# Kernel optimization log

Hardware: AMD Instinct MI355X
Metric: run time of the kernel (lower is better)

## Reference

```python
import jax, jax.numpy as jnp
import numpy as np

NP, NA = 200000, 100000      # paper / author node counts
E = 1000000                  # edges per relation
DP, DA, H = 128, 64, 32      # paper feat, author feat, hidden


def setup_inputs() -> dict:
    key = jax.random.key(0)
    ks = jax.random.split(key, 22)
    g = lambda k, s: jax.random.normal(k, s, jnp.float32) * 0.05
    z = lambda n: jnp.zeros((n,), jnp.float32)
    return dict(
        x_paper=jax.random.normal(ks[0], (NP, DP), jnp.float32),
        x_author=jax.random.normal(ks[1], (NA, DA), jnp.float32),
        ei_cites=jax.random.randint(ks[2], (2, E), 0, NP),  # paper -> paper
        ei_writes=jnp.stack([jax.random.randint(ks[3], (E,), 0, NA),
                             jax.random.randint(ks[4], (E,), 0, NP)]),  # author -> paper
        ei_rev=jnp.stack([jax.random.randint(ks[5], (E,), 0, NP),
                          jax.random.randint(ks[6], (E,), 0, NA)]),  # paper -> author
        # layer 1 SAGEConv weights per edge type: lin_l (with bias), lin_r (no bias)
        W1l_cites=g(ks[7], (DP, H)), b1l_cites=z(H), W1r_cites=g(ks[8], (DP, H)),
        W1l_writes=g(ks[9], (DA, H)), b1l_writes=z(H), W1r_writes=g(ks[10], (DP, H)),
        W1l_rev=g(ks[11], (DP, H)), b1l_rev=z(H), W1r_rev=g(ks[12], (DA, H)),
        # layer 2
        W2l_cites=g(ks[13], (H, H)), b2l_cites=z(H), W2r_cites=g(ks[14], (H, H)),
        W2l_writes=g(ks[15], (H, H)), b2l_writes=z(H), W2r_writes=g(ks[16], (H, H)),
        W2l_rev=g(ks[17], (H, H)), b2l_rev=z(H), W2r_rev=g(ks[18], (H, H)),
        # head Linear(32, 1)
        Wh=g(ks[19], (H, 1)), bh=z(1),
    )


def _sage(x_src, x_dst, ei, Wl, bl, Wr):
    """SAGEConv: lin_l(mean_{j in N(i)} x_j) + lin_r(x_i)."""
    n_dst = x_dst.shape[0]
    src, dst = ei[0], ei[1]
    msum = jax.ops.segment_sum(x_src[src], dst, num_segments=n_dst)  # [n_dst, d_src]
    cnt = jax.ops.segment_sum(jnp.ones((ei.shape[1],), x_src.dtype), dst,
                              num_segments=n_dst)
    mean = msum / jnp.maximum(cnt, 1.0)[:, None]  # zero-degree rows stay 0
    return mean @ Wl + bl + x_dst @ Wr


def reference(x_paper, x_author, ei_cites, ei_writes, ei_rev,
              W1l_cites, b1l_cites, W1r_cites,
              W1l_writes, b1l_writes, W1r_writes,
              W1l_rev, b1l_rev, W1r_rev,
              W2l_cites, b2l_cites, W2r_cites,
              W2l_writes, b2l_writes, W2r_writes,
              W2l_rev, b2l_rev, W2r_rev,
              Wh, bh):
    # layer 1 (to_hetero: sum over edge types per dst node type), then relu
    p1 = jax.nn.relu(_sage(x_paper, x_paper, ei_cites, W1l_cites, b1l_cites, W1r_cites)
                     + _sage(x_author, x_paper, ei_writes, W1l_writes, b1l_writes, W1r_writes))
    a1 = jax.nn.relu(_sage(x_paper, x_author, ei_rev, W1l_rev, b1l_rev, W1r_rev))
    # layer 2: only the 'paper' output is consumed downstream
    p2 = (_sage(p1, p1, ei_cites, W2l_cites, b2l_cites, W2r_cites)
          + _sage(a1, p1, ei_writes, W2l_writes, b2l_writes, W2r_writes))
    # head: Linear(32, 1); model_config is None -> raw logits
    return p2 @ Wh + bh
```

## Files before the change

kernel.cpp:

```cpp
#include <hip/hip_runtime.h>
#include <hip/hip_bf16.h>


#define SPAN  2048
#define EPT   8
#define NBKT  1563
#define CAP   1024
#define SMASK 0x3FFFF

typedef __bf16 bf16x8 __attribute__((ext_vector_type(8)));
typedef __bf16 bf16x2 __attribute__((ext_vector_type(2)));
typedef float f32x4 __attribute__((ext_vector_type(4)));

__global__ void prep_kernel(const float* W1l_c, const float* W1l_rev,
                            const float* W1r_c, const float* W1r_w,
                            const float* W1l_w, const float* W1r_rev,
                            const float* W2l_c, const float* W2l_w,
                            const float* W2r_c, const float* W2r_w,
                            const float* b2l_c, const float* b2l_w,
                            const float* Wh, const float* bh,
                            __bf16* Bp_t, __bf16* Ba_t, float* uvec, int* gcur) {
    int t = threadIdx.x;
    for (int i = t; i < 3 * NBKT; i += 256) gcur[i] = i << 10;
    for (int idx = t; idx < 96 * 128; idx += 256) {
        int n = idx >> 7, k = idx & 127;
        float v;
        if (n < 32)      v = W1l_c[k * 32 + n];
        else if (n < 64) v = W1l_rev[k * 32 + (n - 32)];
        else             v = W1r_c[k * 32 + (n - 64)] + W1r_w[k * 32 + (n - 64)];
        Bp_t[n * 128 + k] = (__bf16)v;
    }
    for (int idx = t; idx < 64 * 64; idx += 256) {
        int n = idx >> 6, k = idx & 63;
        float v = (n < 32) ? W1l_w[k * 32 + n] : W1r_rev[k * 32 + (n - 32)];
        Ba_t[n * 64 + k] = (__bf16)v;
    }
    if (t < 32) {
        float uc = 0.f, uw = 0.f, ur = 0.f;
        for (int j = 0; j < 32; ++j) {
            float wh = Wh[j];
            uc += W2l_c[t * 32 + j] * wh;
            uw += W2l_w[t * 32 + j] * wh;
            ur += (W2r_c[t * 32 + j] + W2r_w[t * 32 + j]) * wh;
        }
        uvec[t] = uc; uvec[32 + t] = uw; uvec[64 + t] = ur;
        if (t == 0) {
            float c0 = bh[0];
            for (int j = 0; j < 32; ++j) c0 += (b2l_c[j] + b2l_w[j]) * Wh[j];
            uvec[96] = c0;
        }
    }
}

template <int K, int NG>
__device__ __forceinline__ void proj_body(const float* __restrict__ X,
                                          const __bf16* __restrict__ Bt,
                                          __bf16* __restrict__ D0,
                                          __bf16* __restrict__ D1,
                                          __bf16* __restrict__ D2, int M, int bid) {
    constexpr int NT = NG * 2, KT = K / 32;
    int lane = threadIdx.x & 63;
    int wave = (bid * 256 + (int)threadIdx.x) >> 6;
    int m0 = wave * 16;
    if (m0 + 16 > M) return;
    int lr = lane & 15;
    int quad = lane >> 4;

    bf16x8 bfrag[NT][KT];
#pragma unroll
    for (int ct = 0; ct < NT; ++ct)
#pragma unroll
        for (int ks = 0; ks < KT; ++ks)
            bfrag[ct][ks] = *(const bf16x8*)(Bt + (ct * 16 + lr) * K + ks * 32 + quad * 8);

    bf16x8 afrag[KT];
    const float* xrow = X + (size_t)(m0 + lr) * K + quad * 8;
#pragma unroll
    for (int ks = 0; ks < KT; ++ks) {
        f32x4 lo = *(const f32x4*)(xrow + ks * 32);
        f32x4 hi = *(const f32x4*)(xrow + ks * 32 + 4);
        bf16x8 a;
#pragma unroll
        for (int j = 0; j < 4; ++j) { a[j] = (__bf16)lo[j]; a[4 + j] = (__bf16)hi[j]; }
        afrag[ks] = a;
    }

    int odd = lane & 1;
#pragma unroll
    for (int ct = 0; ct < NT; ++ct) {
        f32x4 acc = {0.f, 0.f, 0.f, 0.f};
#pragma unroll
        for (int ks = 0; ks < KT; ++ks)
            acc = __builtin_amdgcn_mfma_f32_16x16x32_bf16(afrag[ks], bfrag[ct][ks], acc, 0, 0, 0);
        __bf16* D = ((ct >> 1) == 0) ? D0 : (((ct >> 1) == 1) ? D1 : D2);
        int col = (ct & 1) * 16 + lr;
        int cw = col & ~1;
        int rbase = m0 + quad * 4;
        float o0 = __shfl_xor(acc[0], 1, 64);
        float o1 = __shfl_xor(acc[1], 1, 64);
        float o2 = __shfl_xor(acc[2], 1, 64);
        float o3 = __shfl_xor(acc[3], 1, 64);
        float s0 = odd ? o2 : acc[0], t0 = odd ? acc[2] : o0;
        float s1 = odd ? o3 : acc[1], t1 = odd ? acc[3] : o1;
        int rb = rbase + odd * 2;
        bf16x2 v0; v0[0] = (__bf16)s0; v0[1] = (__bf16)t0;
        bf16x2 v1; v1[0] = (__bf16)s1; v1[1] = (__bf16)t1;
        *(bf16x2*)(D + (size_t)(rb + 0) * 32 + cw) = v0;
        *(bf16x2*)(D + (size_t)(rb + 1) * 32 + cw) = v1;
    }
}

__device__ void scatter_body(const int* __restrict__ eiC, const int* __restrict__ eiW,
                             const int* __restrict__ eiR, int* __restrict__ gcur,
                             unsigned* __restrict__ ebuf, int E, int npart, int bid,
                             int* cnt) {
    int rel = bid / npart, blk = bid % npart;
    const int* ei = rel == 0 ? eiC : (rel == 1 ? eiW : eiR);
    int shift = (rel == 2) ? 6 : 7;
    unsigned dmask = (1u << shift) - 1;
    int t = threadIdx.x;
    int e0 = blk * SPAN, e1 = min(E, e0 + SPAN);
    for (int i = t; i < NBKT; i += 256) cnt[i] = 0;
    __syncthreads();
    int d8[EPT], s8[EPT];
#pragma unroll
    for (int j = 0; j < EPT; ++j) {
        int e = e0 + t + j * 256;
        if (e < e1) {
            d8[j] = ei[E + e];
            s8[j] = ei[e];
            atomicAdd(&cnt[d8[j] >> shift], 1);
        } else {
            d8[j] = -1;
        }
    }
    __syncthreads();
    for (int i = t; i < NBKT; i += 256) {
        int c = cnt[i];
        cnt[i] = c ? atomicAdd(&gcur[rel * NBKT + i], c) : 0;
    }
    __syncthreads();
#pragma unroll
    for (int j = 0; j < EPT; ++j) {
        if (d8[j] >= 0) {
            int b = d8[j] >> shift;
            int gpos = atomicAdd(&cnt[b], 1);
            if (gpos < (((rel * NBKT + b) + 1) << 10))
                ebuf[gpos] = ((unsigned)(d8[j] & dmask) << 18) | (unsigned)s8[j];
        }
    }
}

__global__ __launch_bounds__(256) void mid_kernel(
    const float* __restrict__ Xp, const float* __restrict__ Xa,
    const __bf16* __restrict__ Bp_t, const __bf16* __restrict__ Ba_t,
    __bf16* __restrict__ YpC, __bf16* __restrict__ YpR, __bf16* __restrict__ YpD,
    __bf16* __restrict__ YaW, __bf16* __restrict__ YaD,
    const int* __restrict__ eiC, const int* __restrict__ eiW,
    const int* __restrict__ eiR, int* __restrict__ gcur,
    unsigned* __restrict__ ebuf, int NP, int NA, int E,
    int nPp, int nPa, int npart) {
    __shared__ int cnt[NBKT];
    int bid = blockIdx.x;
    if (bid < 3 * npart) {
        scatter_body(eiC, eiW, eiR, gcur, ebuf, E, npart, bid, cnt);
        return;
    }
    bid -= 3 * npart;
    if (bid < nPp) { proj_body<128, 3>(Xp, Bp_t, YpC, YpR, YpD, NP, bid); return; }
    bid -= nPp;
    proj_body<64, 2>(Xa, Ba_t, YaW, YaD, nullptr, NA, bid);
}

__global__ __launch_bounds__(256) void sort_kernel(
    unsigned* __restrict__ ebuf, const int* __restrict__ gcur,
    int* __restrict__ nstart, int* __restrict__ ncnt) {
    __shared__ unsigned stage[CAP];
    __shared__ int cnt[128], exc[128], cur[128];
    int idx = blockIdx.x;
    int rel = idx / NBKT, b = idx % NBKT;
    int nodes = (rel == 2) ? 64 : 128;
    int t = threadIdx.x;
    int start = idx << 10;
    int n = min(gcur[idx] - start, CAP);
    if (t < 128) cnt[t] = 0;
    __syncthreads();
    for (int i = t; i < n; i += 256) atomicAdd(&cnt[ebuf[start + i] >> 18], 1);
    __syncthreads();
    if (t < 128) exc[t] = cnt[t];
    __syncthreads();
    for (int d = 1; d < 128; d <<= 1) {
        int v = 0;
        if (t < 128) v = exc[t] + ((t >= d) ? exc[t - d] : 0);
        __syncthreads();
        if (t < 128) exc[t] = v;
        __syncthreads();
    }
    if (t < 128) { int e = exc[t] - cnt[t]; exc[t] = e; cur[t] = e; }
    __syncthreads();
    for (int i = t; i < n; i += 256) {
        unsigned w = ebuf[start + i];
        int pos = atomicAdd(&cur[w >> 18], 1);
        stage[pos] = w & SMASK;
    }
    __syncthreads();
    for (int i = t; i < n; i += 256) ebuf[start + i] = stage[i];
    int nbase = (rel == 0) ? b * 128
              : (rel == 1) ? NBKT * 128 + b * 128
                           : 2 * NBKT * 128 + b * 64;
    if (t < nodes) { nstart[nbase + t] = start + exc[t]; ncnt[nbase + t] = cnt[t]; }
}

__device__ __forceinline__ float2 gather2(const __bf16* __restrict__ S,
                                          const unsigned* __restrict__ ebuf,
                                          int o, int n, int l16, int sub) {
    float x = 0.f, y = 0.f;
    int e = sub;
    for (; e + 6 < n; e += 8) {
        int s0 = ebuf[o + e], s1 = ebuf[o + e + 2];
        int s2 = ebuf[o + e + 4], s3 = ebuf[o + e + 6];
        bf16x2 v0 = *(const bf16x2*)(S + (size_t)s0 * 32 + 2 * l16);
        bf16x2 v1 = *(const bf16x2*)(S + (size_t)s1 * 32 + 2 * l16);
        bf16x2 v2 = *(const bf16x2*)(S + (size_t)s2 * 32 + 2 * l16);
        bf16x2 v3 = *(const bf16x2*)(S + (size_t)s3 * 32 + 2 * l16);
        x += (float)v0[0] + (float)v1[0] + (float)v2[0] + (float)v3[0];
        y += (float)v0[1] + (float)v1[1] + (float)v2[1] + (float)v3[1];
    }
    for (; e < n; e += 2) {
        bf16x2 v = *(const bf16x2*)(S + (size_t)ebuf[o + e] * 32 + 2 * l16);
        x += (float)v[0]; y += (float)v[1];
    }
    x += __shfl_xor(x, 16, 64);
    y += __shfl_xor(y, 16, 64);
    return make_float2(x, y);
}

__global__ __launch_bounds__(256) void agg_kernel(
    const __bf16* __restrict__ YpC, const __bf16* __restrict__ YaW,
    const __bf16* __restrict__ YpD, const __bf16* __restrict__ YpR,
    const __bf16* __restrict__ YaD, const unsigned* __restrict__ ebuf,
    const int* __restrict__ nstart, const int* __restrict__ ncnt,
    const float* __restrict__ b1l_c, const float* __restrict__ b1l_w,
    const float* __restrict__ b1l_r, const float* __restrict__ uvec,
    float* __restrict__ s_c, float* __restrict__ s_r, float* __restrict__ s_w,
    int NP, int NA) {
    int g = (blockIdx.x * 256 + (int)threadIdx.x) >> 5;
    int lane32 = threadIdx.x & 31;
    int l16 = lane32 & 15, sub = lane32 >> 4, c2 = 2 * l16;
    const int NPS = NBKT * 128;
    if (g < NP) {
        int oC = nstart[g], nC = ncnt[g];
        float2 aC = gather2(YpC, ebuf, oC, nC, l16, sub);
        int oW = nstart[NPS + g], nW = ncnt[NPS + g];
        float2 aW = gather2(YaW, ebuf, oW, nW, l16, sub);
        float rC = 1.f / (float)max(nC, 1), rW = 1.f / (float)max(nW, 1);
        bf16x2 d = *(const bf16x2*)(YpD + (size_t)g * 32 + c2);
        float p0 = fmaxf(aC.x * rC + aW.x * rW + (float)d[0] + b1l_c[c2] + b1l_w[c2], 0.f);
        float p1 = fmaxf(aC.y * rC + aW.y * rW + (float)d[1] + b1l_c[c2 + 1] + b1l_w[c2 + 1], 0.f);
        float vc = p0 * uvec[c2] + p1 * uvec[c2 + 1];
        float vr = p0 * uvec[64 + c2] + p1 * uvec[64 + c2 + 1];
        for (int m = 1; m < 16; m <<= 1) {
            vc += __shfl_xor(vc, m, 64); vr += __shfl_xor(vr, m, 64);
        }
        if (lane32 == 0) { s_c[g] = vc; s_r[g] = vr; }
    } else if (g < NP + NA) {
        int ga = g - NP;
        int oR = nstart[2 * NPS + ga], nR = ncnt[2 * NPS + ga];
        float2 aR = gather2(YpR, ebuf, oR, nR, l16, sub);
        float rR = 1.f / (float)max(nR, 1);
        bf16x2 d = *(const bf16x2*)(YaD + (size_t)ga * 32 + c2);
        float p0 = fmaxf(aR.x * rR + (float)d[0] + b1l_r[c2], 0.f);
        float p1 = fmaxf(aR.y * rR + (float)d[1] + b1l_r[c2 + 1], 0.f);
        float vw = p0 * uvec[32 + c2] + p1 * uvec[32 + c2 + 1];
        for (int m = 1; m < 16; m <<= 1) vw += __shfl_xor(vw, m, 64);
        if (lane32 == 0) s_w[ga] = vw;
    }
}

__global__ __launch_bounds__(256) void out_kernel(
    const float* __restrict__ s_c, const float* __restrict__ s_w,
    const float* __restrict__ s_r, const unsigned* __restrict__ ebuf,
    const int* __restrict__ nstart, const int* __restrict__ ncnt,
    const float* __restrict__ uvec, float* __restrict__ out, int NP) {
    int gn = blockIdx.x * 256 + threadIdx.x;
    if (gn >= NP) return;
    const int NPS = NBKT * 128;
    int o = nstart[gn], n = ncnt[gn];
    float sC = 0.f;
    for (int e = 0; e < n; ++e) sC += s_c[ebuf[o + e]];
    int o2 = nstart[NPS + gn], n2 = ncnt[NPS + gn];
    float sW = 0.f;
    for (int e = 0; e < n2; ++e) sW += s_w[ebuf[o2 + e]];
    out[gn] = sC / (float)max(n, 1) + sW / (float)max(n2, 1) + s_r[gn] + uvec[96];
}

extern "C" void kernel_launch(void* const* d_in, const int* in_sizes, int n_in,
                              void* d_out, int out_size, void* d_ws, size_t ws_size,
                              hipStream_t stream) {
    const float* x_paper  = (const float*)d_in[0];
    const float* x_author = (const float*)d_in[1];
    const int* eiC = (const int*)d_in[2];
    const int* eiW = (const int*)d_in[3];
    const int* eiR = (const int*)d_in[4];
    const float* W1l_c  = (const float*)d_in[5];
    const float* b1l_c  = (const float*)d_in[6];
    const float* W1r_c  = (const float*)d_in[7];
    const float* W1l_w  = (const float*)d_in[8];
    const float* b1l_w  = (const float*)d_in[9];
    const float* W1r_w  = (const float*)d_in[10];
    const float* W1l_r  = (const float*)d_in[11];
    const float* b1l_r  = (const float*)d_in[12];
    const float* W1r_r  = (const float*)d_in[13];
    const float* W2l_c  = (const float*)d_in[14];
    const float* b2l_c  = (const float*)d_in[15];
    const float* W2r_c  = (const float*)d_in[16];
    const float* W2l_w  = (const float*)d_in[17];
    const float* b2l_w  = (const float*)d_in[18];
    const float* W2r_w  = (const float*)d_in[19];
    const float* Wh = (const float*)d_in[23];
    const float* bh = (const float*)d_in[24];

    const int NP = in_sizes[0] / 128;
    const int NA = in_sizes[1] / 64;
    const int E  = in_sizes[2] / 2;
    const int npart = (E + SPAN - 1) / SPAN;
    const int nPp = (NP + 63) / 64;
    const int nPa = (NA + 63) / 64;
    const int NNODE = NBKT * 128 * 2 + NBKT * 64;

    char* p = (char*)d_ws;
    auto alloc = [&](size_t bytes) -> void* {
        void* r = (void*)p;
        p += (bytes + 255) & ~(size_t)255;
        return r;
    };
    __bf16* YpC = (__bf16*)alloc((size_t)NP * 32 * 2);
    __bf16* YpR = (__bf16*)alloc((size_t)NP * 32 * 2);
    __bf16* YpD = (__bf16*)alloc((size_t)NP * 32 * 2);
    __bf16* YaW = (__bf16*)alloc((size_t)NA * 32 * 2);
    __bf16* YaD = (__bf16*)alloc((size_t)NA * 32 * 2);
    __bf16* Bp_t = (__bf16*)alloc(96 * 128 * 2);
    __bf16* Ba_t = (__bf16*)alloc(64 * 64 * 2);
    float* uvec = (float*)alloc(128 * 4);
    float* s_c  = (float*)alloc((size_t)NP * 4);
    float* s_r  = (float*)alloc((size_t)NP * 4);
    float* s_w  = (float*)alloc((size_t)NA * 4);
    int* gcur   = (int*)alloc((size_t)3 * NBKT * 4);
    int* nstart = (int*)alloc((size_t)NNODE * 4);
    int* ncnt   = (int*)alloc((size_t)NNODE * 4);
    unsigned* ebuf = (unsigned*)alloc((size_t)3 * NBKT * CAP * 4);

    prep_kernel<<<1, 256, 0, stream>>>(W1l_c, W1l_r, W1r_c, W1r_w, W1l_w, W1r_r,
                                       W2l_c, W2l_w, W2r_c, W2r_w, b2l_c, b2l_w,
                                       Wh, bh, Bp_t, Ba_t, uvec, gcur);

    mid_kernel<<<nPp + nPa + 3 * npart, 256, 0, stream>>>(
        x_paper, x_author, Bp_t, Ba_t, YpC, YpR, YpD, YaW, YaD,
        eiC, eiW, eiR, gcur, ebuf, NP, NA, E, nPp, nPa, npart);

    sort_kernel<<<3 * NBKT, 256, 0, stream>>>(ebuf, gcur, nstart, ncnt);

    agg_kernel<<<((NP + NA) * 32 + 255) / 256, 256, 0, stream>>>(
        YpC, YaW, YpD, YpR, YaD, ebuf, nstart, ncnt,
        b1l_c, b1l_w, b1l_r, uvec, s_c, s_r, s_w, NP, NA);

    out_kernel<<<(NP + 255) / 256, 256, 0, stream>>>(
        s_c, s_w, s_r, ebuf, nstart, ncnt, uvec, (float*)d_out, NP);
}
```

Baseline: 436.1 us.

## Fuse bucket sort with layer-1 aggregation using LDS-resident sorted edge lists

Merges the per-bucket counting sort and the layer-1 gather/aggregate into one kernel. Each block sorts its cites and writes buckets (or one rev bucket) in shared memory and reads neighbor indices straight from LDS instead of re-reading the sorted global edge buffer. The rev relation is no longer written back to global memory because only layer 1 uses it. Gather loops now process four edges per iteration with predicated tails, in both the fused kernel and the final output kernel. This removes one kernel launch and a global round trip of the edge lists, at the cost of 16 lanes per node instead of 32 and lower per-block parallelism.

```diff
diff --git a/kernel.cpp b/kernel.cpp
--- a/kernel.cpp
+++ b/kernel.cpp
@@ -172,108 +172,152 @@
     proj_body<64, 2>(Xa, Ba_t, YaW, YaD, nullptr, NA, bid);
 }
 
-__global__ __launch_bounds__(256) void sort_kernel(
-    unsigned* __restrict__ ebuf, const int* __restrict__ gcur,
-    int* __restrict__ nstart, int* __restrict__ ncnt) {
-    __shared__ unsigned stage[CAP];
-    __shared__ int cnt[128], exc[128], cur[128];
-    int idx = blockIdx.x;
-    int rel = idx / NBKT, b = idx % NBKT;
-    int nodes = (rel == 2) ? 64 : 128;
-    int t = threadIdx.x;
-    int start = idx << 10;
-    int n = min(gcur[idx] - start, CAP);
-    if (t < 128) cnt[t] = 0;
-    __syncthreads();
-    for (int i = t; i < n; i += 256) atomicAdd(&cnt[ebuf[start + i] >> 18], 1);
-    __syncthreads();
-    if (t < 128) exc[t] = cnt[t];
-    __syncthreads();
-    for (int d = 1; d < 128; d <<= 1) {
-        int v = 0;
-        if (t < 128) v = exc[t] + ((t >= d) ? exc[t - d] : 0);
-        __syncthreads();
-        if (t < 128) exc[t] = v;
-        __syncthreads();
-    }
-    if (t < 128) { int e = exc[t] - cnt[t]; exc[t] = e; cur[t] = e; }
-    __syncthreads();
-    for (int i = t; i < n; i += 256) {
-        unsigned w = ebuf[start + i];
-        int pos = atomicAdd(&cur[w >> 18], 1);
-        stage[pos] = w & SMASK;
-    }
-    __syncthreads();
-    for (int i = t; i < n; i += 256) ebuf[start + i] = stage[i];
-    int nbase = (rel == 0) ? b * 128
-              : (rel == 1) ? NBKT * 128 + b * 128
-                           : 2 * NBKT * 128 + b * 64;
-    if (t < nodes) { nstart[nbase + t] = start + exc[t]; ncnt[nbase + t] = cnt[t]; }
-}
-
-__device__ __forceinline__ float2 gather2(const __bf16* __restrict__ S,
-                                          const unsigned* __restrict__ ebuf,
-                                          int o, int n, int l16, int sub) {
+__device__ __forceinline__ float2 gatherL(const __bf16* __restrict__ S,
+                                          const unsigned* __restrict__ lst,
+                                          int o, int n, int l16) {
     float x = 0.f, y = 0.f;
-    int e = sub;
-    for (; e + 6 < n; e += 8) {
-        int s0 = ebuf[o + e], s1 = ebuf[o + e + 2];
-        int s2 = ebuf[o + e + 4], s3 = ebuf[o + e + 6];
+    for (int e = 0; e < n; e += 4) {
+        int m = n - e;
+        unsigned s0 = lst[o + e];
+        unsigned s1 = (m > 1) ? lst[o + e + 1] : s0;
+        unsigned s2 = (m > 2) ? lst[o + e + 2] : s0;
+        unsigned s3 = (m > 3) ? lst[o + e + 3] : s0;
         bf16x2 v0 = *(const bf16x2*)(S + (size_t)s0 * 32 + 2 * l16);
         bf16x2 v1 = *(const bf16x2*)(S + (size_t)s1 * 32 + 2 * l16);
         bf16x2 v2 = *(const bf16x2*)(S + (size_t)s2 * 32 + 2 * l16);
         bf16x2 v3 = *(const bf16x2*)(S + (size_t)s3 * 32 + 2 * l16);
-        x += (float)v0[0] + (float)v1[0] + (float)v2[0] + (float)v3[0];
-        y += (float)v0[1] + (float)v1[1] + (float)v2[1] + (float)v3[1];
-    }
-    for (; e < n; e += 2) {
-        bf16x2 v = *(const bf16x2*)(S + (size_t)ebuf[o + e] * 32 + 2 * l16);
-        x += (float)v[0]; y += (float)v[1];
-    }
-    x += __shfl_xor(x, 16, 64);
-    y += __shfl_xor(y, 16, 64);
+        x += (float)v0[0]; y += (float)v0[1];
+        if (m > 1) { x += (float)v1[0]; y += (float)v1[1]; }
+        if (m > 2) { x += (float)v2[0]; y += (float)v2[1]; }
+        if (m > 3) { x += (float)v3[0]; y += (float)v3[1]; }
+    }
     return make_float2(x, y);
 }
 
-__global__ __launch_bounds__(256) void agg_kernel(
+__global__ __launch_bounds__(256) void sagg_kernel(
     const __bf16* __restrict__ YpC, const __bf16* __restrict__ YaW,
     const __bf16* __restrict__ YpD, const __bf16* __restrict__ YpR,
-    const __bf16* __restrict__ YaD, const unsigned* __restrict__ ebuf,
-    const int* __restrict__ nstart, const int* __restrict__ ncnt,
+    const __bf16* __restrict__ YaD, unsigned* __restrict__ ebuf,
+    const int* __restrict__ gcur, int* __restrict__ nstart, int* __restrict__ ncnt,
     const float* __restrict__ b1l_c, const float* __restrict__ b1l_w,
     const float* __restrict__ b1l_r, const float* __restrict__ uvec,
     float* __restrict__ s_c, float* __restrict__ s_r, float* __restrict__ s_w,
     int NP, int NA) {
-    int g = (blockIdx.x * 256 + (int)threadIdx.x) >> 5;
-    int lane32 = threadIdx.x & 31;
-    int l16 = lane32 & 15, sub = lane32 >> 4, c2 = 2 * l16;
+    __shared__ unsigned S0[CAP], S1[CAP];
+    __shared__ int cnt0[128], exc0[128], cur0[128];
+    __shared__ int cnt1[128], exc1[128], cur1[128];
+    __shared__ int scan[256];
     const int NPS = NBKT * 128;
-    if (g < NP) {
-        int oC = nstart[g], nC = ncnt[g];
-        float2 aC = gather2(YpC, ebuf, oC, nC, l16, sub);
-        int oW = nstart[NPS + g], nW = ncnt[NPS + g];
-        float2 aW = gather2(YaW, ebuf, oW, nW, l16, sub);
-        float rC = 1.f / (float)max(nC, 1), rW = 1.f / (float)max(nW, 1);
-        bf16x2 d = *(const bf16x2*)(YpD + (size_t)g * 32 + c2);
-        float p0 = fmaxf(aC.x * rC + aW.x * rW + (float)d[0] + b1l_c[c2] + b1l_w[c2], 0.f);
-        float p1 = fmaxf(aC.y * rC + aW.y * rW + (float)d[1] + b1l_c[c2 + 1] + b1l_w[c2 + 1], 0.f);
-        float vc = p0 * uvec[c2] + p1 * uvec[c2 + 1];
-        float vr = p0 * uvec[64 + c2] + p1 * uvec[64 + c2 + 1];
-        for (int m = 1; m < 16; m <<= 1) {
-            vc += __shfl_xor(vc, m, 64); vr += __shfl_xor(vr, m, 64);
-        }
-        if (lane32 == 0) { s_c[g] = vc; s_r[g] = vr; }
-    } else if (g < NP + NA) {
-        int ga = g - NP;
-        int oR = nstart[2 * NPS + ga], nR = ncnt[2 * NPS + ga];
-        float2 aR = gather2(YpR, ebuf, oR, nR, l16, sub);
-        float rR = 1.f / (float)max(nR, 1);
-        bf16x2 d = *(const bf16x2*)(YaD + (size_t)ga * 32 + c2);
-        float p0 = fmaxf(aR.x * rR + (float)d[0] + b1l_r[c2], 0.f);
-        float p1 = fmaxf(aR.y * rR + (float)d[1] + b1l_r[c2 + 1], 0.f);
-        float vw = p0 * uvec[32 + c2] + p1 * uvec[32 + c2 + 1];
-        for (int m = 1; m < 16; m <<= 1) vw += __shfl_xor(vw, m, 64);
-        if (lane32 == 0) s_w[ga] = vw;
+    int t = threadIdx.x;
+    int sg = t >> 4, l16 = t & 15, c2 = 2 * l16;
+    int bid = blockIdx.x;
+
+    if (bid < NBKT) {
+        int b = bid;
+        int i0 = b, i1 = NBKT + b;
+        int st0 = i0 << 10, st1 = i1 << 10;
+        int n0 = min(gcur[i0] - st0, CAP), n1 = min(gcur[i1] - st1, CAP);
+        if (t < 128) { cnt0[t] = 0; cnt1[t] = 0; }
+        __syncthreads();
+        for (int i = t; i < n0; i += 256) atomicAdd(&cnt0[ebuf[st0 + i] >> 18], 1);
+        for (int i = t; i < n1; i += 256) atomicAdd(&cnt1[ebuf[st1 + i] >> 18], 1);
+        __syncthreads();
+        int own = (t < 128) ? cnt0[t] : cnt1[t - 128];
+        scan[t] = own;
+        __syncthreads();
+        for (int d = 1; d < 128; d <<= 1) {
+            int nv = scan[t] + (((t & 127) >= d) ? scan[t - d] : 0);
+            __syncthreads();
+            scan[t] = nv;
+            __syncthreads();
+        }
+        int excl = scan[t] - own;
+        if (t < 128) { exc0[t] = excl; cur0[t] = excl; }
+        else         { exc1[t - 128] = excl; cur1[t - 128] = excl; }
+        __syncthreads();
+        for (int i = t; i < n0; i += 256) {
+            unsigned w = ebuf[st0 + i];
+            int pos = atomicAdd(&cur0[w >> 18], 1);
+            S0[pos] = w & SMASK;
+        }
+        for (int i = t; i < n1; i += 256) {
+            unsigned w = ebuf[st1 + i];
+            int pos = atomicAdd(&cur1[w >> 18], 1);
+            S1[pos] = w & SMASK;
+        }
+        __syncthreads();
+        for (int i = t; i < n0; i += 256) ebuf[st0 + i] = S0[i];
+        for (int i = t; i < n1; i += 256) ebuf[st1 + i] = S1[i];
+        if (t < 128) {
+            nstart[b * 128 + t] = st0 + exc0[t];
+            ncnt[b * 128 + t] = cnt0[t];
+            nstart[NPS + b * 128 + t] = st1 + exc1[t];
+            ncnt[NPS + b * 128 + t] = cnt1[t];
+        }
+        float u0 = uvec[c2], u1 = uvec[c2 + 1];
+        float w0 = uvec[64 + c2], w1 = uvec[64 + c2 + 1];
+        float bc0 = b1l_c[c2] + b1l_w[c2], bc1 = b1l_c[c2 + 1] + b1l_w[c2 + 1];
+        for (int k = 0; k < 8; ++k) {
+            int nd = sg * 8 + k;
+            int g = b * 128 + nd;
+            if (g >= NP) break;
+            int nC = cnt0[nd], nW = cnt1[nd];
+            float2 aC = gatherL(YpC, S0, exc0[nd], nC, l16);
+            float2 aW = gatherL(YaW, S1, exc1[nd], nW, l16);
+            float rC = 1.f / (float)max(nC, 1), rW = 1.f / (float)max(nW, 1);
+            bf16x2 d = *(const bf16x2*)(YpD + (size_t)g * 32 + c2);
+            float p0 = fmaxf(aC.x * rC + aW.x * rW + (float)d[0] + bc0, 0.f);
+            float p1 = fmaxf(aC.y * rC + aW.y * rW + (float)d[1] + bc1, 0.f);
+            float vc = p0 * u0 + p1 * u1;
+            float vr = p0 * w0 + p1 * w1;
+            for (int m = 1; m < 16; m <<= 1) {
+                vc += __shfl_xor(vc, m, 64); vr += __shfl_xor(vr, m, 64);
+            }
+            if (l16 == 0) { s_c[g] = vc; s_r[g] = vr; }
+        }
+    } else {
+        int b = bid - NBKT;
+        int i2 = 2 * NBKT + b;
+        int st2 = i2 << 10;
+        int n2 = min(gcur[i2] - st2, CAP);
+        if (t < 128) { cnt0[t] = 0; cnt1[t] = 0; }
+        __syncthreads();
+        for (int i = t; i < n2; i += 256) atomicAdd(&cnt0[ebuf[st2 + i] >> 18], 1);
+        __syncthreads();
+        int own = (t < 128) ? cnt0[t] : 0;
+        scan[t] = own;
+        __syncthreads();
+        for (int d = 1; d < 128; d <<= 1) {
+            int nv = scan[t] + (((t & 127) >= d) ? scan[t - d] : 0);
+            __syncthreads();
+            scan[t] = nv;
+            __syncthreads();
+        }
+        int excl = scan[t] - own;
+        if (t < 128) { exc0[t] = excl; cur0[t] = excl; }
+        __syncthreads();
+        for (int i = t; i < n2; i += 256) {
+            unsigned w = ebuf[st2 + i];
+            int pos = atomicAdd(&cur0[w >> 18], 1);
+            S0[pos] = w & SMASK;
+        }
+        __syncthreads();
+        float uw0 = uvec[32 + c2], uw1 = uvec[32 + c2 + 1];
+        float br0 = b1l_r[c2], br1 = b1l_r[c2 + 1];
+        for (int k = 0; k < 4; ++k) {
+            int nd = sg * 4 + k;
+            int ga = b * 64 + nd;
+            if (ga >= NA) break;
+            int nR = cnt0[nd];
+            float2 aR = gatherL(YpR, S0, exc0[nd], nR, l16);
+            float rR = 1.f / (float)max(nR, 1);
+            bf16x2 d = *(const bf16x2*)(YaD + (size_t)ga * 32 + c2);
+            float p0 = fmaxf(aR.x * rR + (float)d[0] + br0, 0.f);
+            float p1 = fmaxf(aR.y * rR + (float)d[1] + br1, 0.f);
+            float vw = p0 * uw0 + p1 * uw1;
+            for (int m = 1; m < 16; m <<= 1) vw += __shfl_xor(vw, m, 64);
+            if (l16 == 0) s_w[ga] = vw;
+        }
     }
 }
 
@@ -287,10 +331,32 @@
     const int NPS = NBKT * 128;
     int o = nstart[gn], n = ncnt[gn];
     float sC = 0.f;
-    for (int e = 0; e < n; ++e) sC += s_c[ebuf[o + e]];
+    for (int e = 0; e < n; e += 4) {
+        int m = n - e;
+        int a0 = ebuf[o + e];
+        int a1 = (m > 1) ? (int)ebuf[o + e + 1] : a0;
+        int a2 = (m > 2) ? (int)ebuf[o + e + 2] : a0;
+        int a3 = (m > 3) ? (int)ebuf[o + e + 3] : a0;
+        float f0 = s_c[a0], f1 = s_c[a1], f2 = s_c[a2], f3 = s_c[a3];
+        sC += f0;
+        if (m > 1) sC += f1;
+        if (m > 2) sC += f2;
+        if (m > 3) sC += f3;
+    }
     int o2 = nstart[NPS + gn], n2 = ncnt[NPS + gn];
     float sW = 0.f;
-    for (int e = 0; e < n2; ++e) sW += s_w[ebuf[o2 + e]];
+    for (int e = 0; e < n2; e += 4) {
+        int m = n2 - e;
+        int a0 = ebuf[o2 + e];
+        int a1 = (m > 1) ? (int)ebuf[o2 + e + 1] : a0;
+        int a2 = (m > 2) ? (int)ebuf[o2 + e + 2] : a0;
+        int a3 = (m > 3) ? (int)ebuf[o2 + e + 3] : a0;
+        float f0 = s_w[a0], f1 = s_w[a1], f2 = s_w[a2], f3 = s_w[a3];
+        sW += f0;
+        if (m > 1) sW += f1;
+        if (m > 2) sW += f2;
+        if (m > 3) sW += f3;
+    }
     out[gn] = sC / (float)max(n, 1) + sW / (float)max(n2, 1) + s_r[gn] + uvec[96];
 }
 
@@ -358,10 +424,8 @@
         x_paper, x_author, Bp_t, Ba_t, YpC, YpR, YpD, YaW, YaD,
         eiC, eiW, eiR, gcur, ebuf, NP, NA, E, nPp, nPa, npart);
 
-    sort_kernel<<<3 * NBKT, 256, 0, stream>>>(ebuf, gcur, nstart, ncnt);
-
-    agg_kernel<<<((NP + NA) * 32 + 255) / 256, 256, 0, stream>>>(
-        YpC, YaW, YpD, YpR, YaD, ebuf, nstart, ncnt,
+    sagg_kernel<<<2 * NBKT, 256, 0, stream>>>(
+        YpC, YaW, YpD, YpR, YaD, ebuf, gcur, nstart, ncnt,
         b1l_c, b1l_w, b1l_r, uvec, s_c, s_r, s_w, NP, NA);
 
     out_kernel<<<(NP + 255) / 256, 256, 0, stream>>>(
```

New measurement: 398.1 us (median of 2 runs). 8.7% less time.
